# Kernel optimization log

Measured on AMD Instinct MI355X. Metric: run time of the kernel, lower is better.

Reference implementation:

```python
import jax, jax.numpy as jnp
import numpy as np

N_USERS = 100000
N_ITEMS = 50000
N_NODES = N_USERS + N_ITEMS
N_EDGES = 4800000
EMB_DIM = 64
N_LAYERS = 3


def setup_inputs() -> dict:
    key = jax.random.key(0)
    k1, k2, k3, k4, k5 = jax.random.split(key, 5)
    user_emb = jax.random.normal(k1, (N_USERS, EMB_DIM), dtype=jnp.float32)
    item_emb = jax.random.normal(k2, (N_ITEMS, EMB_DIM), dtype=jnp.float32)
    # COO representation of the (symmetric-normalized) adjacency matrix
    edge_src = jax.random.randint(k3, (N_EDGES,), 0, N_NODES, dtype=jnp.int32)
    edge_dst = jax.random.randint(k4, (N_EDGES,), 0, N_NODES, dtype=jnp.int32)
    edge_weight = jax.random.uniform(k5, (N_EDGES,), dtype=jnp.float32)
    return {
        "user_emb": user_emb,
        "item_emb": item_emb,
        "edge_weight": edge_weight,
        "edge_src": edge_src,
        "edge_dst": edge_dst,
    }


def _spmm(edge_src, edge_dst, edge_weight, x):
    # out[i] = sum_j A[i, j] * x[j]  with A in COO (dst=row i, src=col j)
    msgs = edge_weight[:, None] * x[edge_src]  # [E, D]
    return jax.ops.segment_sum(msgs, edge_dst, num_segments=N_NODES)


def reference(user_emb, item_emb, edge_weight, edge_src, edge_dst):
    ego = jnp.concatenate([user_emb, item_emb], axis=0)  # [N, D]
    acc = ego  # running sum over layer embeddings (layer 0 included)
    for _ in range(N_LAYERS):
        ego = _spmm(edge_src, edge_dst, edge_weight, ego)
        acc = acc + ego
    mean_emb = acc / jnp.float32(N_LAYERS + 1)  # mean over (L+1) layers
    new_user = mean_emb[:N_USERS]
    new_item = mean_emb[N_USERS:]
    return new_user, new_item
```

## Files before the change

### kernel.cpp

```cpp
#include <hip/hip_runtime.h>
#include <hip/hip_fp16.h>

#define N_USERS 100000
#define N_ITEMS 50000
#define N_NODES 150000
#define N_EDGES 4800000
#define EMB 64
#define N_LAYERS 3

#define NBKT 256
#define NPB  586
#define NREP 8
#define SUBCAP 2624
#define CAP (NREP * SUBCAP)

typedef unsigned int u32;
typedef unsigned short u16;
typedef u32 vu4 __attribute__((ext_vector_type(4)));
typedef u32 vu2 __attribute__((ext_vector_type(2)));

#define W_BITS 14
#define W_SCALE 16384.0f
#define W_INV   (1.0f / 16384.0f)
#define W_MASK  16383u

__device__ __forceinline__ float2 h2f(u32 v) {
    float2 r;
    r.x = __half2float(__ushort_as_half((u16)(v & 0xffffu)));
    r.y = __half2float(__ushort_as_half((u16)(v >> 16)));
    return r;
}

__global__ void k_init(const float4* __restrict__ user,
                       const float4* __restrict__ item,
                       ushort4* __restrict__ cur) {
    int i = blockIdx.x * blockDim.x + threadIdx.x;
    const int total4 = N_NODES * EMB / 4;
    const int user4  = N_USERS * EMB / 4;
    if (i >= total4) return;
    float4 v = (i < user4) ? user[i] : item[i - user4];
    ushort4 h;
    h.x = __half_as_ushort(__float2half_rn(v.x));
    h.y = __half_as_ushort(__float2half_rn(v.y));
    h.z = __half_as_ushort(__float2half_rn(v.z));
    h.w = __half_as_ushort(__float2half_rn(v.w));
    cur[i] = h;
}

__global__ __launch_bounds__(256) void k_p1(const int4*   __restrict__ src4,
                                            const int4*   __restrict__ dst4,
                                            const float4* __restrict__ w4,
                                            int* __restrict__ cursor,
                                            u32* __restrict__ pk_arr,
                                            u16* __restrict__ ld_arr) {
    __shared__ int hist[NBKT];
    __shared__ int base[NBKT];
    int tid = threadIdx.x;
    hist[tid] = 0;
    __syncthreads();

    int g0 = blockIdx.x * 512 + tid * 2;
    bool act = (g0 < N_EDGES / 4);

    u32 pk[8];
    u32 meta[8];
    if (act) {
        int4 d0 = dst4[g0], d1 = dst4[g0 + 1];
        int4 s0 = src4[g0], s1 = src4[g0 + 1];
        float4 f0 = w4[g0], f1 = w4[g0 + 1];
        int   ds[8] = {d0.x, d0.y, d0.z, d0.w, d1.x, d1.y, d1.z, d1.w};
        int   ss[8] = {s0.x, s0.y, s0.z, s0.w, s1.x, s1.y, s1.z, s1.w};
        float wf[8] = {f0.x, f0.y, f0.z, f0.w, f1.x, f1.y, f1.z, f1.w};
        #pragma unroll
        for (int k = 0; k < 8; ++k) {
            u32 d  = (u32)ds[k];
            u32 b  = d / NPB;
            u32 ld = d - b * NPB;
            int r  = atomicAdd(&hist[b], 1);
            u32 wq = (u32)(wf[k] * W_SCALE + 0.5f);
            if (wq > W_MASK) wq = W_MASK;
            pk[k]   = ((u32)ss[k] << W_BITS) | wq;
            meta[k] = ((u32)r << 18) | (b << 10) | ld;
        }
    }
    __syncthreads();

    int rep = blockIdx.x & (NREP - 1);
    int h = hist[tid];
    if (h > 0) base[tid] = atomicAdd(&cursor[rep * NBKT + tid], h);
    __syncthreads();

    if (act) {
        #pragma unroll
        for (int k = 0; k < 8; ++k) {
            u32 b  = (meta[k] >> 10) & 255u;
            u32 r  = meta[k] >> 18;
            u32 ld = meta[k] & 1023u;
            int pos = base[b] + (int)r;
            if (pos < SUBCAP) {
                size_t slot = (size_t)b * CAP + (size_t)rep * SUBCAP + pos;
                pk_arr[slot] = pk[k];
                ld_arr[slot] = (u16)ld;
            }
        }
    }
}

__global__ void k_scan256(const int* __restrict__ cursor,
                          int* __restrict__ bkt_base,
                          int* __restrict__ row_ptr) {
    __shared__ int tmp[NBKT];
    int tid = threadIdx.x;
    int tot = 0;
    for (int r = 0; r < NREP; ++r) tot += cursor[r * NBKT + tid];
    tmp[tid] = tot;
    __syncthreads();
    for (int off = 1; off < NBKT; off <<= 1) {
        int t = 0;
        if (tid >= off) t = tmp[tid - off];
        __syncthreads();
        if (tid >= off) tmp[tid] += t;
        __syncthreads();
    }
    bkt_base[tid] = tmp[tid] - tot;
    if (tid == 0) row_ptr[N_NODES] = N_EDGES;
}

__global__ __launch_bounds__(1024) void k_p2(const int* __restrict__ cursor,
                                             const int* __restrict__ bkt_base,
                                             const u32* __restrict__ pk_arr,
                                             const u16* __restrict__ ld_arr,
                                             int* __restrict__ row_ptr,
                                             u32* __restrict__ pairs) {
    __shared__ int hist[1024];
    __shared__ int cur[NPB];
    int b = blockIdx.x;
    int tid = threadIdx.x;
    hist[tid] = 0;
    __syncthreads();

    int lo = b * NPB;
    int nb = N_NODES - lo; if (nb > NPB) nb = NPB;

    int n[NREP];
    #pragma unroll
    for (int r = 0; r < NREP; ++r) {
        int c = cursor[r * NBKT + b];
        n[r] = (c > SUBCAP) ? SUBCAP : c;
    }

    for (int r = 0; r < NREP; ++r) {
        const u16* p = ld_arr + (size_t)b * CAP + (size_t)r * SUBCAP;
        for (int i = tid; i < n[r]; i += 1024)
            atomicAdd(&hist[p[i]], 1);
    }
    __syncthreads();

    int val = hist[tid];
    for (int off = 1; off < 1024; off <<= 1) {
        int t = 0;
        if (tid >= off) t = hist[tid - off];
        __syncthreads();
        if (tid >= off) hist[tid] += t;
        __syncthreads();
    }
    int excl = hist[tid] - val;
    int gbase = bkt_base[b];
    if (tid < nb) {
        row_ptr[lo + tid] = gbase + excl;
        cur[tid] = excl;
    }
    __syncthreads();

    for (int r = 0; r < NREP; ++r) {
        const u16* p = ld_arr + (size_t)b * CAP + (size_t)r * SUBCAP;
        const u32* q = pk_arr + (size_t)b * CAP + (size_t)r * SUBCAP;
        for (int i = tid; i < n[r]; i += 1024) {
            int ld  = p[i];
            int pos = atomicAdd(&cur[ld], 1);
            pairs[gbase + pos] = q[i];
        }
    }
}

struct Dec4 { u32 r0, r1, r2, r3; float w0, w1, w2, w3; };

__device__ __forceinline__ Dec4 dec_fast(vu4 p) {
    Dec4 d;
    d.r0 = p.x >> W_BITS; d.w0 = (float)(p.x & W_MASK) * W_INV;
    d.r1 = p.y >> W_BITS; d.w1 = (float)(p.y & W_MASK) * W_INV;
    d.r2 = p.z >> W_BITS; d.w2 = (float)(p.z & W_MASK) * W_INV;
    d.r3 = p.w >> W_BITS; d.w3 = (float)(p.w & W_MASK) * W_INV;
    return d;
}

__device__ __forceinline__ Dec4 dec_mask(vu4 p, int eb, int beg, int end) {
    Dec4 d;
    bool v0 = (eb + 0 >= beg) && (eb + 0 < end);
    bool v1 = (eb + 1 >= beg) && (eb + 1 < end);
    bool v2 = (eb + 2 >= beg) && (eb + 2 < end);
    bool v3 = (eb + 3 >= beg) && (eb + 3 < end);
    d.r0 = v0 ? (p.x >> W_BITS) : 0u; d.w0 = v0 ? (float)(p.x & W_MASK) * W_INV : 0.f;
    d.r1 = v1 ? (p.y >> W_BITS) : 0u; d.w1 = v1 ? (float)(p.y & W_MASK) * W_INV : 0.f;
    d.r2 = v2 ? (p.z >> W_BITS) : 0u; d.w2 = v2 ? (float)(p.z & W_MASK) * W_INV : 0.f;
    d.r3 = v3 ? (p.w >> W_BITS) : 0u; d.w3 = v3 ? (float)(p.w & W_MASK) * W_INV : 0.f;
    return d;
}

__device__ __forceinline__ Dec4 dec(vu4 p, int lo, int beg, int end, int g) {
    if (lo >= beg && lo + 16 <= end) return dec_fast(p);
    return dec_mask(p, lo + 4 * g, beg, end);
}

__device__ __forceinline__ vu2 ldx(const char* xbase, u32 r, u32 moff) {
    return *(const vu2*)(xbase + (size_t)(r * 128u + moff));
}

__device__ __forceinline__ void acc4(vu2 xv, float w,
                                     float& ax, float& ay, float& az, float& aw) {
    float2 lo = h2f(xv.x);
    float2 hi = h2f(xv.y);
    ax = fmaf(w, lo.x, ax); ay = fmaf(w, lo.y, ay);
    az = fmaf(w, hi.x, az); aw = fmaf(w, hi.y, aw);
}

#define LOADX(pfx, d) \
    vu2 pfx##0 = ldx(xbase, d.r0, moff), pfx##1 = ldx(xbase, d.r1, moff), \
        pfx##2 = ldx(xbase, d.r2, moff), pfx##3 = ldx(xbase, d.r3, moff)
#define ACCX(pfx, d) \
    acc4(pfx##0, d.w0, ax, ay, az, aw); acc4(pfx##1, d.w1, ax, ay, az, aw); \
    acc4(pfx##2, d.w2, ax, ay, az, aw); acc4(pfx##3, d.w3, ax, ay, az, aw)

__global__ __launch_bounds__(256) void k_gather(const int* __restrict__ row_ptr,
                                                const u32* __restrict__ pairs,
                                                const __half* __restrict__ x,
                                                __half* __restrict__ nxt) {
    int wave = (blockIdx.x * blockDim.x + threadIdx.x) >> 6;
    int lane = threadIdx.x & 63;
    if (wave >= N_NODES) return;
    int beg = row_ptr[wave];
    int end = row_ptr[wave + 1];

    const int g = lane >> 4;
    const u32 moff = (u32)(lane & 15) << 3;
    const char* xbase = (const char*)x;

    float ax = 0.f, ay = 0.f, az = 0.f, aw = 0.f;

    int jb = beg & ~3;
    int nb = (end - jb + 15) >> 4;
    const u32* pp = pairs + jb + 4 * g;

    if (nb == 1) {
        vu4 P0 = __builtin_nontemporal_load((const vu4*)pp);
        Dec4 d0 = dec(P0, jb, beg, end, g);
        LOADX(xa, d0);
        ACCX(xa, d0);
    } else if (nb == 2) {
        vu4 P0 = __builtin_nontemporal_load((const vu4*)pp);
        vu4 P1 = __builtin_nontemporal_load((const vu4*)(pp + 16));
        Dec4 d0 = dec(P0, jb, beg, end, g);
        LOADX(xa, d0);
        Dec4 d1 = dec(P1, jb + 16, beg, end, g);
        LOADX(xc, d1);
        ACCX(xa, d0);
        ACCX(xc, d1);
    } else if (nb == 3) {
        vu4 P0 = __builtin_nontemporal_load((const vu4*)pp);
        vu4 P1 = __builtin_nontemporal_load((const vu4*)(pp + 16));
        vu4 P2 = __builtin_nontemporal_load((const vu4*)(pp + 32));
        Dec4 d0 = dec(P0, jb, beg, end, g);
        LOADX(xa, d0);
        Dec4 d1 = dec(P1, jb + 16, beg, end, g);
        LOADX(xc, d1);
        ACCX(xa, d0);
        Dec4 d2 = dec(P2, jb + 32, beg, end, g);
        LOADX(xd, d2);
        ACCX(xc, d1);
        ACCX(xd, d2);
    } else if (nb >= 4) {
        vu4 P0 = __builtin_nontemporal_load((const vu4*)pp);
        vu4 P1 = __builtin_nontemporal_load((const vu4*)(pp + 16));
        vu4 P2 = __builtin_nontemporal_load((const vu4*)(pp + 32));
        Dec4 d0 = dec(P0, jb, beg, end, g);
        LOADX(xa, d0);
        Dec4 d1 = dec(P1, jb + 16, beg, end, g);
        LOADX(xc, d1);
        ACCX(xa, d0);
        vu4 P3 = __builtin_nontemporal_load((const vu4*)(pp + 48));
        Dec4 d2 = dec(P2, jb + 32, beg, end, g);
        LOADX(xd, d2);
        ACCX(xc, d1);
        Dec4 d3 = dec(P3, jb + 48, beg, end, g);
        LOADX(xe, d3);
        ACCX(xd, d2);
        ACCX(xe, d3);
        for (int b = 4; b < nb; ++b) {
            vu4 Pl = __builtin_nontemporal_load((const vu4*)(pp + (size_t)16 * b));
            Dec4 dl = dec(Pl, jb + 16 * b, beg, end, g);
            LOADX(xf, dl);
            ACCX(xf, dl);
        }
    }

    ax += __shfl_xor(ax, 16); ax += __shfl_xor(ax, 32);
    ay += __shfl_xor(ay, 16); ay += __shfl_xor(ay, 32);
    az += __shfl_xor(az, 16); az += __shfl_xor(az, 32);
    aw += __shfl_xor(aw, 16); aw += __shfl_xor(aw, 32);

    if (lane < 16) {
        ushort4 h;
        h.x = __half_as_ushort(__float2half_rn(ax));
        h.y = __half_as_ushort(__float2half_rn(ay));
        h.z = __half_as_ushort(__float2half_rn(az));
        h.w = __half_as_ushort(__float2half_rn(aw));
        ((ushort4*)nxt)[(size_t)wave * 16 + (lane & 15)] = h;
    }
}

__global__ void k_fin(const float4* __restrict__ user,
                      const float4* __restrict__ item,
                      const ushort4* __restrict__ e1,
                      const ushort4* __restrict__ e2,
                      const ushort4* __restrict__ e3,
                      float4* __restrict__ out) {
    int i = blockIdx.x * blockDim.x + threadIdx.x;
    const int total4 = N_NODES * EMB / 4;
    const int user4  = N_USERS * EMB / 4;
    if (i >= total4) return;
    float4 v = (i < user4) ? user[i] : item[i - user4];
    ushort4 a = e1[i], b = e2[i], c = e3[i];
    v.x = (v.x + __half2float(__ushort_as_half(a.x))
              + __half2float(__ushort_as_half(b.x))
              + __half2float(__ushort_as_half(c.x))) * 0.25f;
    v.y = (v.y + __half2float(__ushort_as_half(a.y))
              + __half2float(__ushort_as_half(b.y))
              + __half2float(__ushort_as_half(c.y))) * 0.25f;
    v.z = (v.z + __half2float(__ushort_as_half(a.z))
              + __half2float(__ushort_as_half(b.z))
              + __half2float(__ushort_as_half(c.z))) * 0.25f;
    v.w = (v.w + __half2float(__ushort_as_half(a.w))
              + __half2float(__ushort_as_half(b.w))
              + __half2float(__ushort_as_half(c.w))) * 0.25f;
    __builtin_nontemporal_store(v.x, &((float*)out)[4 * (size_t)i + 0]);
    __builtin_nontemporal_store(v.y, &((float*)out)[4 * (size_t)i + 1]);
    __builtin_nontemporal_store(v.z, &((float*)out)[4 * (size_t)i + 2]);
    __builtin_nontemporal_store(v.w, &((float*)out)[4 * (size_t)i + 3]);
}

__global__ void k_spmm(const int*   __restrict__ src,
                       const int*   __restrict__ dst,
                       const float* __restrict__ w,
                       const float* __restrict__ x,
                       float*       __restrict__ y) {
    long long t = (long long)blockIdx.x * blockDim.x + threadIdx.x;
    int e = (int)(t >> 4);
    if (e >= N_EDGES) return;
    int q = (int)(t & 15);
    int   s  = src[e];
    int   d  = dst[e];
    float we = w[e];
    const float4* xs = (const float4*)(x + (long long)s * EMB);
    float4 v = xs[q];
    float* yd = y + (long long)d * EMB + q * 4;
    atomicAdd(yd + 0, we * v.x);
    atomicAdd(yd + 1, we * v.y);
    atomicAdd(yd + 2, we * v.z);
    atomicAdd(yd + 3, we * v.w);
}

__global__ void k_init_f32(const float4* __restrict__ user,
                           const float4* __restrict__ item,
                           float4* __restrict__ out,
                           float4* __restrict__ cur) {
    int i = blockIdx.x * blockDim.x + threadIdx.x;
    const int total4 = N_NODES * EMB / 4;
    const int user4  = N_USERS * EMB / 4;
    if (i >= total4) return;
    float4 v = (i < user4) ? user[i] : item[i - user4];
    out[i] = v;
    cur[i] = v;
}

__global__ void k_acc(float4* __restrict__ out,
                      const float4* __restrict__ buf,
                      float scale) {
    int i = blockIdx.x * blockDim.x + threadIdx.x;
    const int total4 = N_NODES * EMB / 4;
    if (i >= total4) return;
    float4 o = out[i];
    float4 b = buf[i];
    o.x = (o.x + b.x) * scale;
    o.y = (o.y + b.y) * scale;
    o.z = (o.z + b.z) * scale;
    o.w = (o.w + b.w) * scale;
    out[i] = o;
}

extern "C" void kernel_launch(void* const* d_in, const int* in_sizes, int n_in,
                              void* d_out, int out_size, void* d_ws, size_t ws_size,
                              hipStream_t stream) {
    const float* user_emb = (const float*)d_in[0];
    const float* item_emb = (const float*)d_in[1];
    const float* edge_w   = (const float*)d_in[2];
    const int*   edge_src = (const int*)d_in[3];
    const int*   edge_dst = (const int*)d_in[4];
    float* out = (float*)d_out;

    const size_t feat_elems = (size_t)N_NODES * EMB;
    const size_t feat_bytes_f32 = feat_elems * 4;
    const size_t feat_bytes_f16 = feat_elems * 2;

    char* ws = (char*)d_ws;
    size_t off = 0;
    __half* h0 = (__half*)(ws + off); off += feat_bytes_f16;
    __half* h1 = (__half*)(ws + off); off += feat_bytes_f16;
    __half* h2 = (__half*)(ws + off); off += feat_bytes_f16;
    __half* h3 = (__half*)(ws + off); off += feat_bytes_f16;
    int* row_ptr  = (int*)(ws + off); off += ((size_t)(N_NODES + 1) * 4 + 63) / 64 * 64;
    int* cursor   = (int*)(ws + off); off += (size_t)NREP * NBKT * 4;
    int* bkt_base = (int*)(ws + off); off += (size_t)NBKT * 4;
    u32* pk_arr = (u32*)(ws + off);   off += (size_t)NBKT * CAP * 4;
    u16* ld_arr = (u16*)(ws + off);   off += (size_t)NBKT * CAP * 2;
    u32* pairs  = (u32*)(ws + off);   off += (size_t)N_EDGES * 4 + 64;
    const size_t needed = off;

    const int block = 256;
    const int total4 = (int)(feat_elems / 4);
    const int fgrid = (total4 + block - 1) / block;
    const int p1grid = (N_EDGES / 8 + block - 1) / block;
    const int ggrid = (N_NODES + 3) / 4;

    if (ws_size >= needed) {
        (void)hipMemsetAsync(cursor, 0, (size_t)NREP * NBKT * 4, stream);

        k_init<<<fgrid, block, 0, stream>>>((const float4*)user_emb,
                                            (const float4*)item_emb,
                                            (ushort4*)h0);

        k_p1<<<p1grid, block, 0, stream>>>((const int4*)edge_src,
                                           (const int4*)edge_dst,
                                           (const float4*)edge_w,
                                           cursor, pk_arr, ld_arr);
        k_scan256<<<1, NBKT, 0, stream>>>(cursor, bkt_base, row_ptr);
        k_p2<<<NBKT, 1024, 0, stream>>>(cursor, bkt_base, pk_arr, ld_arr,
                                        row_ptr, pairs);

        __half* bufs[4] = {h0, h1, h2, h3};
        for (int layer = 0; layer < N_LAYERS; ++layer)
            k_gather<<<ggrid, block, 0, stream>>>(row_ptr, pairs,
                                                  bufs[layer], bufs[layer + 1]);

        k_fin<<<fgrid, block, 0, stream>>>((const float4*)user_emb,
                                           (const float4*)item_emb,
                                           (const ushort4*)h1,
                                           (const ushort4*)h2,
                                           (const ushort4*)h3,
                                           (float4*)out);
    } else {
        float* buf0 = (float*)d_ws;
        float* buf1 = buf0 + feat_elems;
        k_init_f32<<<fgrid, block, 0, stream>>>((const float4*)user_emb,
                                                (const float4*)item_emb,
                                                (float4*)out, (float4*)buf0);
        float* cur = buf0;
        float* nxt = buf1;
        for (int layer = 0; layer < N_LAYERS; ++layer) {
            (void)hipMemsetAsync(nxt, 0, feat_bytes_f32, stream);
            long long threads = (long long)N_EDGES * 16;
            int grid = (int)((threads + block - 1) / block);
            k_spmm<<<grid, block, 0, stream>>>(edge_src, edge_dst, edge_w, cur, nxt);
            float scale = (layer == N_LAYERS - 1) ? (1.0f / (N_LAYERS + 1)) : 1.0f;
            k_acc<<<fgrid, block, 0, stream>>>((float4*)out, (const float4*)nxt, scale);
            float* tmp = cur; cur = nxt; nxt = tmp;
        }
    }
}
```

Measured before the change: 472.5 us.

## Fuse final averaging into last gather, fold scan into p2, use fma_mix

Removes the separate k_fin pass by computing the layer mean inside the third gather kernel, which avoids writing and re-reading the last-layer fp16 buffer. The 256-bucket scan moves into every k_p2 block, and the cursor memset moves into k_init, which removes two launches. The fp16-to-fp32 convert plus FMA in the inner accumulate becomes a single v_fma_mix_f32 inline asm instruction. The cost is a redundant scan in each p2 block and extra loads at the start of the final gather.

```diff
diff --git a/kernel.cpp b/kernel.cpp
--- a/kernel.cpp
+++ b/kernel.cpp
@@ -18,6 +18,7 @@
 typedef unsigned short u16;
 typedef u32 vu4 __attribute__((ext_vector_type(4)));
 typedef u32 vu2 __attribute__((ext_vector_type(2)));
+typedef float vf4 __attribute__((ext_vector_type(4)));
 
 #define W_BITS 14
 #define W_SCALE 16384.0f
@@ -33,10 +34,12 @@
 
 __global__ void k_init(const float4* __restrict__ user,
                        const float4* __restrict__ item,
-                       ushort4* __restrict__ cur) {
+                       ushort4* __restrict__ cur,
+                       int* __restrict__ cursor) {
     int i = blockIdx.x * blockDim.x + threadIdx.x;
     const int total4 = N_NODES * EMB / 4;
     const int user4  = N_USERS * EMB / 4;
+    if (i < NREP * NBKT) cursor[i] = 0;
     if (i >= total4) return;
     float4 v = (i < user4) ? user[i] : item[i - user4];
     ushort4 h;
@@ -106,38 +109,35 @@
     }
 }
 
-__global__ void k_scan256(const int* __restrict__ cursor,
-                          int* __restrict__ bkt_base,
-                          int* __restrict__ row_ptr) {
-    __shared__ int tmp[NBKT];
-    int tid = threadIdx.x;
-    int tot = 0;
-    for (int r = 0; r < NREP; ++r) tot += cursor[r * NBKT + tid];
-    tmp[tid] = tot;
-    __syncthreads();
-    for (int off = 1; off < NBKT; off <<= 1) {
-        int t = 0;
-        if (tid >= off) t = tmp[tid - off];
-        __syncthreads();
-        if (tid >= off) tmp[tid] += t;
-        __syncthreads();
-    }
-    bkt_base[tid] = tmp[tid] - tot;
-    if (tid == 0) row_ptr[N_NODES] = N_EDGES;
-}
-
 __global__ __launch_bounds__(1024) void k_p2(const int* __restrict__ cursor,
-                                             const int* __restrict__ bkt_base,
                                              const u32* __restrict__ pk_arr,
                                              const u16* __restrict__ ld_arr,
                                              int* __restrict__ row_ptr,
                                              u32* __restrict__ pairs) {
     __shared__ int hist[1024];
     __shared__ int cur[NPB];
+    __shared__ int btot[NBKT];
+    __shared__ int bsum[NBKT];
     int b = blockIdx.x;
     int tid = threadIdx.x;
     hist[tid] = 0;
-    __syncthreads();
+    if (tid < NBKT) {
+        int s = 0;
+        #pragma unroll
+        for (int r = 0; r < NREP; ++r) s += cursor[r * NBKT + tid];
+        btot[tid] = s;
+        bsum[tid] = s;
+    }
+    if (b == 0 && tid == 0) row_ptr[N_NODES] = N_EDGES;
+    __syncthreads();
+    for (int off = 1; off < NBKT; off <<= 1) {
+        int t = 0;
+        if (tid < NBKT && tid >= off) t = bsum[tid - off];
+        __syncthreads();
+        if (tid < NBKT && tid >= off) bsum[tid] += t;
+        __syncthreads();
+    }
+    int gbase = bsum[b] - btot[b];
 
     int lo = b * NPB;
     int nb = N_NODES - lo; if (nb > NPB) nb = NPB;
@@ -165,7 +165,6 @@
         __syncthreads();
     }
     int excl = hist[tid] - val;
-    int gbase = bkt_base[b];
     if (tid < nb) {
         row_ptr[lo + tid] = gbase + excl;
         cur[tid] = excl;
@@ -216,12 +215,17 @@
     return *(const vu2*)(xbase + (size_t)(r * 128u + moff));
 }
 
+__device__ __forceinline__ void fmix2(float& a0, float& a1, float w, u32 x) {
+    asm("v_fma_mix_f32 %0, %1, %2, %0 op_sel:[0,0,0] op_sel_hi:[0,1,0]"
+        : "+v"(a0) : "v"(w), "v"(x));
+    asm("v_fma_mix_f32 %0, %1, %2, %0 op_sel:[0,1,0] op_sel_hi:[0,1,0]"
+        : "+v"(a1) : "v"(w), "v"(x));
+}
+
 __device__ __forceinline__ void acc4(vu2 xv, float w,
                                      float& ax, float& ay, float& az, float& aw) {
-    float2 lo = h2f(xv.x);
-    float2 hi = h2f(xv.y);
-    ax = fmaf(w, lo.x, ax); ay = fmaf(w, lo.y, ay);
-    az = fmaf(w, hi.x, az); aw = fmaf(w, hi.y, aw);
+    fmix2(ax, ay, w, xv.x);
+    fmix2(az, aw, w, xv.y);
 }
 
 #define LOADX(pfx, d) \
@@ -231,18 +235,36 @@
     acc4(pfx##0, d.w0, ax, ay, az, aw); acc4(pfx##1, d.w1, ax, ay, az, aw); \
     acc4(pfx##2, d.w2, ax, ay, az, aw); acc4(pfx##3, d.w3, ax, ay, az, aw)
 
+template<int FIN>
 __global__ __launch_bounds__(256) void k_gather(const int* __restrict__ row_ptr,
                                                 const u32* __restrict__ pairs,
                                                 const __half* __restrict__ x,
-                                                __half* __restrict__ nxt) {
+                                                __half* __restrict__ nxt,
+                                                const float4* __restrict__ user,
+                                                const float4* __restrict__ item,
+                                                const ushort4* __restrict__ e1,
+                                                const ushort4* __restrict__ e2,
+                                                float* __restrict__ outp) {
     int wave = (blockIdx.x * blockDim.x + threadIdx.x) >> 6;
     int lane = threadIdx.x & 63;
     if (wave >= N_NODES) return;
+
+    const int m = lane & 15;
+    float4 ego = {};
+    ushort4 pa = {}, pb = {};
+    if (FIN && lane < 16) {
+        size_t idx = (size_t)wave * 16 + m;
+        const size_t user4 = (size_t)N_USERS * 16;
+        ego = (idx < user4) ? user[idx] : item[idx - user4];
+        pa = e1[idx];
+        pb = e2[idx];
+    }
+
     int beg = row_ptr[wave];
     int end = row_ptr[wave + 1];
 
     const int g = lane >> 4;
-    const u32 moff = (u32)(lane & 15) << 3;
+    const u32 moff = (u32)m << 3;
     const char* xbase = (const char*)x;
 
     float ax = 0.f, ay = 0.f, az = 0.f, aw = 0.f;
@@ -309,43 +331,26 @@
     aw += __shfl_xor(aw, 16); aw += __shfl_xor(aw, 32);
 
     if (lane < 16) {
-        ushort4 h;
-        h.x = __half_as_ushort(__float2half_rn(ax));
-        h.y = __half_as_ushort(__float2half_rn(ay));
-        h.z = __half_as_ushort(__float2half_rn(az));
-        h.w = __half_as_ushort(__float2half_rn(aw));
-        ((ushort4*)nxt)[(size_t)wave * 16 + (lane & 15)] = h;
-    }
-}
-
-__global__ void k_fin(const float4* __restrict__ user,
-                      const float4* __restrict__ item,
-                      const ushort4* __restrict__ e1,
-                      const ushort4* __restrict__ e2,
-                      const ushort4* __restrict__ e3,
-                      float4* __restrict__ out) {
-    int i = blockIdx.x * blockDim.x + threadIdx.x;
-    const int total4 = N_NODES * EMB / 4;
-    const int user4  = N_USERS * EMB / 4;
-    if (i >= total4) return;
-    float4 v = (i < user4) ? user[i] : item[i - user4];
-    ushort4 a = e1[i], b = e2[i], c = e3[i];
-    v.x = (v.x + __half2float(__ushort_as_half(a.x))
-              + __half2float(__ushort_as_half(b.x))
-              + __half2float(__ushort_as_half(c.x))) * 0.25f;
-    v.y = (v.y + __half2float(__ushort_as_half(a.y))
-              + __half2float(__ushort_as_half(b.y))
-              + __half2float(__ushort_as_half(c.y))) * 0.25f;
-    v.z = (v.z + __half2float(__ushort_as_half(a.z))
-              + __half2float(__ushort_as_half(b.z))
-              + __half2float(__ushort_as_half(c.z))) * 0.25f;
-    v.w = (v.w + __half2float(__ushort_as_half(a.w))
-              + __half2float(__ushort_as_half(b.w))
-              + __half2float(__ushort_as_half(c.w))) * 0.25f;
-    __builtin_nontemporal_store(v.x, &((float*)out)[4 * (size_t)i + 0]);
-    __builtin_nontemporal_store(v.y, &((float*)out)[4 * (size_t)i + 1]);
-    __builtin_nontemporal_store(v.z, &((float*)out)[4 * (size_t)i + 2]);
-    __builtin_nontemporal_store(v.w, &((float*)out)[4 * (size_t)i + 3]);
+        if (FIN) {
+            vf4 o;
+            o.x = (ego.x + __half2float(__ushort_as_half(pa.x))
+                         + __half2float(__ushort_as_half(pb.x)) + ax) * 0.25f;
+            o.y = (ego.y + __half2float(__ushort_as_half(pa.y))
+                         + __half2float(__ushort_as_half(pb.y)) + ay) * 0.25f;
+            o.z = (ego.z + __half2float(__ushort_as_half(pa.z))
+                         + __half2float(__ushort_as_half(pb.z)) + az) * 0.25f;
+            o.w = (ego.w + __half2float(__ushort_as_half(pa.w))
+                         + __half2float(__ushort_as_half(pb.w)) + aw) * 0.25f;
+            __builtin_nontemporal_store(o, (vf4*)outp + (size_t)wave * 16 + m);
+        } else {
+            ushort4 h;
+            h.x = __half_as_ushort(__float2half_rn(ax));
+            h.y = __half_as_ushort(__float2half_rn(ay));
+            h.z = __half_as_ushort(__float2half_rn(az));
+            h.w = __half_as_ushort(__float2half_rn(aw));
+            ((ushort4*)nxt)[(size_t)wave * 16 + m] = h;
+        }
+    }
 }
 
 __global__ void k_spmm(const int*   __restrict__ src,
@@ -416,10 +421,8 @@
     __half* h0 = (__half*)(ws + off); off += feat_bytes_f16;
     __half* h1 = (__half*)(ws + off); off += feat_bytes_f16;
     __half* h2 = (__half*)(ws + off); off += feat_bytes_f16;
-    __half* h3 = (__half*)(ws + off); off += feat_bytes_f16;
     int* row_ptr  = (int*)(ws + off); off += ((size_t)(N_NODES + 1) * 4 + 63) / 64 * 64;
     int* cursor   = (int*)(ws + off); off += (size_t)NREP * NBKT * 4;
-    int* bkt_base = (int*)(ws + off); off += (size_t)NBKT * 4;
     u32* pk_arr = (u32*)(ws + off);   off += (size_t)NBKT * CAP * 4;
     u16* ld_arr = (u16*)(ws + off);   off += (size_t)NBKT * CAP * 2;
     u32* pairs  = (u32*)(ws + off);   off += (size_t)N_EDGES * 4 + 64;
@@ -432,31 +435,29 @@
     const int ggrid = (N_NODES + 3) / 4;
 
     if (ws_size >= needed) {
-        (void)hipMemsetAsync(cursor, 0, (size_t)NREP * NBKT * 4, stream);
-
         k_init<<<fgrid, block, 0, stream>>>((const float4*)user_emb,
                                             (const float4*)item_emb,
-                                            (ushort4*)h0);
+                                            (ushort4*)h0, cursor);
 
         k_p1<<<p1grid, block, 0, stream>>>((const int4*)edge_src,
                                            (const int4*)edge_dst,
                                            (const float4*)edge_w,
                                            cursor, pk_arr, ld_arr);
-        k_scan256<<<1, NBKT, 0, stream>>>(cursor, bkt_base, row_ptr);
-        k_p2<<<NBKT, 1024, 0, stream>>>(cursor, bkt_base, pk_arr, ld_arr,
+        k_p2<<<NBKT, 1024, 0, stream>>>(cursor, pk_arr, ld_arr,
                                         row_ptr, pairs);
 
-        __half* bufs[4] = {h0, h1, h2, h3};
-        for (int layer = 0; layer < N_LAYERS; ++layer)
-            k_gather<<<ggrid, block, 0, stream>>>(row_ptr, pairs,
-                                                  bufs[layer], bufs[layer + 1]);
-
-        k_fin<<<fgrid, block, 0, stream>>>((const float4*)user_emb,
-                                           (const float4*)item_emb,
-                                           (const ushort4*)h1,
-                                           (const ushort4*)h2,
-                                           (const ushort4*)h3,
-                                           (float4*)out);
+        k_gather<0><<<ggrid, block, 0, stream>>>(row_ptr, pairs, h0, h1,
+                                                 nullptr, nullptr, nullptr,
+                                                 nullptr, nullptr);
+        k_gather<0><<<ggrid, block, 0, stream>>>(row_ptr, pairs, h1, h2,
+                                                 nullptr, nullptr, nullptr,
+                                                 nullptr, nullptr);
+        k_gather<1><<<ggrid, block, 0, stream>>>(row_ptr, pairs, h2, nullptr,
+                                                 (const float4*)user_emb,
+                                                 (const float4*)item_emb,
+                                                 (const ushort4*)h1,
+                                                 (const ushort4*)h2,
+                                                 out);
     } else {
         float* buf0 = (float*)d_ws;
         float* buf1 = buf0 + feat_elems;
```

After: 465.2 us. No clear change (-1.5%).
